# Kernel optimization log

Measured on AMD Instinct MI355X. Metric: run time of the kernel, lower is better.

The kernel has to match this reference:

```python
import jax, jax.numpy as jnp
import numpy as np

RADIUS = 2  # matches init kwarg

def lga3d(cost, filters, radius):
    """One pass of GANet local guided 3D aggregation.
    cost:    [B, C, D, H, W]
    filters: [B, 3*K*K, H, W], K = 2*radius+1; 3 groups for depth offsets d-1, d, d+1.
    Out-of-range taps (depth or spatial) contribute zero.
    """
    B, C, D, H, W = cost.shape
    K = 2 * radius + 1
    # zero-pad: 1 plane on each side of depth, `radius` on each spatial side
    cp = jnp.pad(cost, ((0, 0), (0, 0), (1, 1), (radius, radius), (radius, radius)))
    out = jnp.zeros_like(cost)
    for g in range(3):            # depth offsets -1, 0, +1
        for i in range(K):        # vertical window offset
            for j in range(K):    # horizontal window offset
                w = filters[:, g * K * K + i * K + j][:, None, None]  # [B,1,1,H,W]
                patch = jax.lax.dynamic_slice(cp, (0, 0, g, i, j), (B, C, D, H, W))
                out = out + w * patch
    return out


def setup_inputs() -> dict:
    key = jax.random.key(0)
    k1, k2 = jax.random.split(key)
    B, C, D, H, W = 1, 16, 48, 128, 256
    K = 2 * RADIUS + 1
    cost = jax.random.normal(k1, (B, C, D, H, W), dtype=jnp.float32)
    filters = jax.random.normal(k2, (B, 3 * K * K, H, W), dtype=jnp.float32) * 0.1
    return {"cost": cost, "filters": filters}


def reference(cost, filters):
    # Lga3d3Function applies the aggregation three times with the same filters.
    out = lga3d(cost, filters, RADIUS)
    out = lga3d(out, filters, RADIUS)
    out = lga3d(out, filters, RADIUS)
    return out
```

## Files before the change

kernel.cpp:

```cpp
#include <hip/hip_runtime.h>


namespace {
constexpr int C  = 16, D = 48, H = 128, W = 256;
constexpr int TH = 4, TW = 64;
constexpr int LH = TH + 4;
constexpr int LW = 72;
constexpr int NF = 75;
constexpr int HW = H * W;
constexpr int SLOTS = LH * (LW / 4);
}

__global__ __launch_bounds__(256, 4)
void lga_pass(const float* __restrict__ in, const float* __restrict__ filt,
              float* __restrict__ out)
{
    __shared__ float buf[2][LH * LW];

    const int tx = threadIdx.x;
    const int ty = threadIdx.y;
    const int tid = ty * 64 + tx;
    const int w0 = blockIdx.x * TW;
    const int h0 = blockIdx.y * TH;
    const int c  = blockIdx.z;
    const int h  = h0 + ty;
    const int w  = w0 + tx;

    float f[NF];
    #pragma unroll
    for (int k = 0; k < NF; ++k)
        f[k] = filt[k * HW + h * W + w];

    const bool haveSlot = tid < SLOTS;
    const int r  = tid / 18;
    const int q  = tid - r * 18;
    const int gh = h0 - 2 + r;
    const int gw = w0 - 4 + 4 * q;
    const bool valid = haveSlot && (gh >= 0) && (gh < H) && (gw >= 0) && (gw < W);
    const int planeOff = gh * W + gw;
    const float* planeBase = in + c * (D * HW);

    for (int k = tid; k < 2 * LH * LW; k += 256)
        (&buf[0][0])[k] = 0.f;
    __syncthreads();

    auto stage = [&](int dp, int bsel) {
        if (valid) {
            __builtin_amdgcn_global_load_lds(
                (const __attribute__((address_space(1))) void*)(planeBase + dp * HW + planeOff),
                (__attribute__((address_space(3))) void*)(&buf[bsel][ty * 256]),
                16, 0, 0);
        }
    };

    stage(0, 0);
    __syncthreads();

    float a_prev = 0.f, a_cur = 0.f;
    float* outp = out + c * (D * HW) + h * W + w;

    for (int d = 0; d < D; ++d) {
        if (d + 1 < D) stage(d + 1, (d + 1) & 1);

        const float* bp = &buf[d & 1][ty * LW + tx + 2];
        float s0 = 0.f, s1 = 0.f, s2 = 0.f;
        #pragma unroll
        for (int i = 0; i < 5; ++i) {
            #pragma unroll
            for (int j = 0; j < 5; ++j) {
                float v = bp[i * LW + j];
                s0 = fmaf(f[     i * 5 + j], v, s0);
                s1 = fmaf(f[25 + i * 5 + j], v, s1);
                s2 = fmaf(f[50 + i * 5 + j], v, s2);
            }
        }

        float done = a_prev + s2;
        if (d > 0) outp[(d - 1) * HW] = done;
        a_prev = a_cur + s1;
        a_cur  = s0;
        __syncthreads();
    }
    outp[(D - 1) * HW] = a_prev;
}

extern "C" void kernel_launch(void* const* d_in, const int* in_sizes, int n_in,
                              void* d_out, int out_size, void* d_ws, size_t ws_size,
                              hipStream_t stream)
{
    const float* cost = (const float*)d_in[0];
    const float* filt = (const float*)d_in[1];
    float* out = (float*)d_out;

    const size_t needBytes = (size_t)C * D * HW * sizeof(float);
    float* tmp = (ws_size >= needBytes) ? (float*)d_ws : (float*)d_in[0];

    dim3 block(64, 4, 1);
    dim3 grid(W / TW, H / TH, C);

    lga_pass<<<grid, block, 0, stream>>>(cost, filt, out);
    lga_pass<<<grid, block, 0, stream>>>(out,  filt, tmp);
    lga_pass<<<grid, block, 0, stream>>>(tmp,  filt, out);
}
```

Baseline: 393.2 us.

## Process two channels per block to reuse per-pixel filter registers

Each block now aggregates two channels instead of one. The 75 filter taps held in registers are reused for both channel planes, and the depth-staged LDS buffer is widened to hold both planes, with a second partial load slot covering the extra 32 vec4s. This halves redundant filter loads and doubles the independent FMA chains per thread. In exchange the grid has half as many blocks, LDS use grows, and the occupancy hint drops from 4 to 3 blocks.

```diff
diff --git a/kernel.cpp b/kernel.cpp
--- a/kernel.cpp
+++ b/kernel.cpp
@@ -7,81 +7,105 @@
 constexpr int LH = TH + 4;
 constexpr int LW = 72;
 constexpr int NF = 75;
-constexpr int HW = H * W;
-constexpr int SLOTS = LH * (LW / 4);
+constexpr int HWp = H * W;
+constexpr int CPB = 2;
+constexpr int CPLANE   = LH * LW;
+constexpr int SLOTS_CH = CPLANE / 4;
+constexpr int SLOTS    = CPB * SLOTS_CH;
+constexpr int BUFHALF  = CPB * CPLANE;
 }
 
-__global__ __launch_bounds__(256, 4)
+__global__ __launch_bounds__(256, 3)
 void lga_pass(const float* __restrict__ in, const float* __restrict__ filt,
               float* __restrict__ out)
 {
-    __shared__ float buf[2][LH * LW];
+    __shared__ float buf[2][CPB][CPLANE];
+    float* bufF = &buf[0][0][0];
 
     const int tx = threadIdx.x;
     const int ty = threadIdx.y;
     const int tid = ty * 64 + tx;
     const int w0 = blockIdx.x * TW;
     const int h0 = blockIdx.y * TH;
-    const int c  = blockIdx.z;
+    const int c0 = blockIdx.z * CPB;
     const int h  = h0 + ty;
     const int w  = w0 + tx;
 
     float f[NF];
     #pragma unroll
     for (int k = 0; k < NF; ++k)
-        f[k] = filt[k * HW + h * W + w];
+        f[k] = filt[k * HWp + h * W + w];
 
-    const bool haveSlot = tid < SLOTS;
-    const int r  = tid / 18;
-    const int q  = tid - r * 18;
-    const int gh = h0 - 2 + r;
-    const int gw = w0 - 4 + 4 * q;
-    const bool valid = haveSlot && (gh >= 0) && (gh < H) && (gw >= 0) && (gw < W);
-    const int planeOff = gh * W + gw;
-    const float* planeBase = in + c * (D * HW);
+    auto geom = [&](int s, bool& valid, long& goff) {
+        const int ch = s / SLOTS_CH;
+        const int sc = s - ch * SLOTS_CH;
+        const int r  = sc / 18;
+        const int q  = sc - r * 18;
+        const int gh = h0 - 2 + r;
+        const int gw = w0 - 4 + 4 * q;
+        valid = (gh >= 0) && (gh < H) && (gw >= 0) && (gw < W);
+        goff  = (long)(c0 + ch) * (D * HWp) + gh * (long)W + gw;
+    };
+    bool validA, validB;
+    long goffA, goffB;
+    geom(tid, validA, goffA);
+    geom(256 + tid, validB, goffB);
 
-    for (int k = tid; k < 2 * LH * LW; k += 256)
-        (&buf[0][0])[k] = 0.f;
+    for (int k = tid; k < 2 * BUFHALF; k += 256)
+        bufF[k] = 0.f;
     __syncthreads();
 
     auto stage = [&](int dp, int bsel) {
-        if (valid) {
+        if (validA)
             __builtin_amdgcn_global_load_lds(
-                (const __attribute__((address_space(1))) void*)(planeBase + dp * HW + planeOff),
-                (__attribute__((address_space(3))) void*)(&buf[bsel][ty * 256]),
+                (const __attribute__((address_space(1))) void*)(in + goffA + (long)dp * HWp),
+                (__attribute__((address_space(3))) void*)(bufF + bsel * BUFHALF + ty * 256),
                 16, 0, 0);
-        }
+        if (tid < 32 && validB)
+            __builtin_amdgcn_global_load_lds(
+                (const __attribute__((address_space(1))) void*)(in + goffB + (long)dp * HWp),
+                (__attribute__((address_space(3))) void*)(bufF + bsel * BUFHALF + 1024),
+                16, 0, 0);
     };
 
     stage(0, 0);
     __syncthreads();
 
-    float a_prev = 0.f, a_cur = 0.f;
-    float* outp = out + c * (D * HW) + h * W + w;
+    float aP0 = 0.f, aC0 = 0.f, aP1 = 0.f, aC1 = 0.f;
+    float* outp0 = out + (long)c0 * (D * HWp) + h * W + w;
+    float* outp1 = outp0 + D * HWp;
 
     for (int d = 0; d < D; ++d) {
         if (d + 1 < D) stage(d + 1, (d + 1) & 1);
 
-        const float* bp = &buf[d & 1][ty * LW + tx + 2];
-        float s0 = 0.f, s1 = 0.f, s2 = 0.f;
+        const float* b0 = bufF + (d & 1) * BUFHALF + ty * LW + tx + 2;
+        const float* b1 = b0 + CPLANE;
+        float s00 = 0.f, s01 = 0.f, s02 = 0.f;
+        float s10 = 0.f, s11 = 0.f, s12 = 0.f;
         #pragma unroll
         for (int i = 0; i < 5; ++i) {
             #pragma unroll
             for (int j = 0; j < 5; ++j) {
-                float v = bp[i * LW + j];
-                s0 = fmaf(f[     i * 5 + j], v, s0);
-                s1 = fmaf(f[25 + i * 5 + j], v, s1);
-                s2 = fmaf(f[50 + i * 5 + j], v, s2);
+                const float v0 = b0[i * LW + j];
+                const float v1 = b1[i * LW + j];
+                const float fa = f[     i * 5 + j];
+                const float fb = f[25 + i * 5 + j];
+                const float fc = f[50 + i * 5 + j];
+                s00 = fmaf(fa, v0, s00); s01 = fmaf(fb, v0, s01); s02 = fmaf(fc, v0, s02);
+                s10 = fmaf(fa, v1, s10); s11 = fmaf(fb, v1, s11); s12 = fmaf(fc, v1, s12);
             }
         }
 
-        float done = a_prev + s2;
-        if (d > 0) outp[(d - 1) * HW] = done;
-        a_prev = a_cur + s1;
-        a_cur  = s0;
+        if (d > 0) {
+            outp0[(d - 1) * HWp] = aP0 + s02;
+            outp1[(d - 1) * HWp] = aP1 + s12;
+        }
+        aP0 = aC0 + s01; aC0 = s00;
+        aP1 = aC1 + s11; aC1 = s10;
         __syncthreads();
     }
-    outp[(D - 1) * HW] = a_prev;
+    outp0[(D - 1) * HWp] = aP0;
+    outp1[(D - 1) * HWp] = aP1;
 }
 
 extern "C" void kernel_launch(void* const* d_in, const int* in_sizes, int n_in,
@@ -92,11 +116,11 @@
     const float* filt = (const float*)d_in[1];
     float* out = (float*)d_out;
 
-    const size_t needBytes = (size_t)C * D * HW * sizeof(float);
+    const size_t needBytes = (size_t)C * D * HWp * sizeof(float);
     float* tmp = (ws_size >= needBytes) ? (float*)d_ws : (float*)d_in[0];
 
     dim3 block(64, 4, 1);
-    dim3 grid(W / TW, H / TH, C);
+    dim3 grid(W / TW, H / TH, C / CPB);
 
     lga_pass<<<grid, block, 0, stream>>>(cost, filt, out);
     lga_pass<<<grid, block, 0, stream>>>(out,  filt, tmp);
```

Result: slower. 575.4 us (+46.3%).
